# Kernel optimization log

Measured on AMD Instinct MI355X. Metric: run time of the kernel, lower is better.

The kernel has to match this reference:

```python
import jax, jax.numpy as jnp
import numpy as np

HIDDEN_DIM = 2048
NUM_HEADS = 16
HEAD_DIM = HIDDEN_DIM // NUM_HEADS
BATCH = 2
SEQ = 2048


def setup_inputs() -> dict:
    key = jax.random.key(0)
    ks = jax.random.split(key, 5)
    scale = 1.0 / np.sqrt(HIDDEN_DIM)
    x = jax.random.normal(ks[0], (BATCH, SEQ, HIDDEN_DIM), dtype=jnp.float32)
    w_q = jax.random.normal(ks[1], (HIDDEN_DIM, HIDDEN_DIM), dtype=jnp.float32) * scale
    w_k = jax.random.normal(ks[2], (HIDDEN_DIM, HIDDEN_DIM), dtype=jnp.float32) * scale
    w_v = jax.random.normal(ks[3], (HIDDEN_DIM, HIDDEN_DIM), dtype=jnp.float32) * scale
    w_o = jax.random.normal(ks[4], (HIDDEN_DIM, HIDDEN_DIM), dtype=jnp.float32) * scale
    return {"x": x, "w_q": w_q, "w_k": w_k, "w_v": w_v, "w_o": w_o}


def reference(x, w_q, w_k, w_v, w_o):
    # Projections: x @ W.T  (weights stored as (out, in) like torch)
    q = jnp.einsum('bsd,ed->bse', x, w_q)
    k = jnp.einsum('bsd,ed->bse', x, w_k)
    v = jnp.einsum('bsd,ed->bse', x, w_v)
    b, s, _ = q.shape
    # split heads: (b, h, s, hd)
    q = q.reshape(b, s, NUM_HEADS, HEAD_DIM).transpose(0, 2, 1, 3)
    k = k.reshape(b, s, NUM_HEADS, HEAD_DIM).transpose(0, 2, 1, 3)
    v = v.reshape(b, s, NUM_HEADS, HEAD_DIM).transpose(0, 2, 1, 3)
    scale = 1.0 / np.sqrt(HEAD_DIM)
    # Online-softmax tiling in the source (causal=False default) is
    # mathematically identical to standard softmax attention.
    scores = jnp.einsum('bhqd,bhkd->bhqk', q, k) * scale
    p = jax.nn.softmax(scores, axis=-1)
    o = jnp.einsum('bhqk,bhkd->bhqd', p, v)
    o = o.transpose(0, 2, 1, 3).reshape(b, s, HIDDEN_DIM)
    return jnp.einsum('bsd,ed->bse', o, w_o)
```

## Files before the change

### kernel.cpp

```cpp
#include <hip/hip_runtime.h>


typedef _Float16 half8 __attribute__((ext_vector_type(8)));
typedef float floatx4 __attribute__((ext_vector_type(4)));

__device__ __forceinline__ void async16(const void* g, void* l) {
  __builtin_amdgcn_global_load_lds((__attribute__((address_space(1))) void*)(g),
                                   (__attribute__((address_space(3))) void*)(l),
                                   16, 0, 0);
}

__global__ void cvt_f32_f16(const float* __restrict__ src, _Float16* __restrict__ dst,
                            int n4) {
  int i = blockIdx.x * blockDim.x + threadIdx.x;
  if (i >= n4) return;
  float4 v = reinterpret_cast<const float4*>(src)[i];
  union { _Float16 h[4]; short4 s; } u;
  u.h[0] = (_Float16)v.x; u.h[1] = (_Float16)v.y;
  u.h[2] = (_Float16)v.z; u.h[3] = (_Float16)v.w;
  reinterpret_cast<short4*>(dst)[i] = u.s;
}

__global__ void cvt_w4(const float* __restrict__ w0, const float* __restrict__ w1,
                       const float* __restrict__ w2, const float* __restrict__ w3,
                       _Float16* __restrict__ dst, float scale0) {
  int i = blockIdx.x * blockDim.x + threadIdx.x;
  int m = i >> 20, j = i & ((1 << 20) - 1);
  const float* src = (m == 0) ? w0 : (m == 1) ? w1 : (m == 2) ? w2 : w3;
  float sc = (m == 0) ? scale0 : 1.0f;
  float4 v = reinterpret_cast<const float4*>(src)[j];
  union { _Float16 h[4]; short4 s; } u;
  u.h[0] = (_Float16)(v.x * sc); u.h[1] = (_Float16)(v.y * sc);
  u.h[2] = (_Float16)(v.z * sc); u.h[3] = (_Float16)(v.w * sc);
  reinterpret_cast<short4*>(dst)[i] = u.s;
}

template <int OUT_MODE>
__global__ __launch_bounds__(256)
void gemm_nt(const _Float16* __restrict__ A, const _Float16* __restrict__ Bw,
             void* __restrict__ Cv, void* __restrict__ Cv2, int K) {
  __shared__ _Float16 As[128 * 64];
  __shared__ _Float16 Bs[128 * 64];
  const int tid = threadIdx.x;
  const int wave = tid >> 6, lane = tid & 63;
  const int wm = wave >> 1, wn = wave & 1;
  const int l15 = lane & 15, l4 = lane >> 4;
  const int bm = blockIdx.y, bn = blockIdx.x;

  floatx4 acc[4][4] = {};

  for (int k0 = 0; k0 < K; k0 += 64) {
    __syncthreads();
#pragma unroll
    for (int i = 0; i < 4; ++i) {
      int c = i * 256 + tid;
      int row = c >> 3, cc = c & 7;
      int g = cc ^ (row & 7);
      async16(A + (size_t)(bm * 128 + row) * K + k0 + g * 8, &As[c * 8]);
      async16(Bw + (size_t)(bn * 128 + row) * K + k0 + g * 8, &Bs[c * 8]);
    }
    __syncthreads();
#pragma unroll
    for (int ks = 0; ks < 2; ++ks) {
      half8 af[4], bf[4];
#pragma unroll
      for (int t = 0; t < 4; ++t) {
        int ra = wm * 64 + t * 16 + l15;
        int rb = wn * 64 + t * 16 + l15;
        int ch = (ks * 4 + l4) ^ (l15 & 7);
        af[t] = *reinterpret_cast<const half8*>(&As[ra * 64 + ch * 8]);
        bf[t] = *reinterpret_cast<const half8*>(&Bs[rb * 64 + ch * 8]);
      }
#pragma unroll
      for (int mt = 0; mt < 4; ++mt)
#pragma unroll
        for (int nt = 0; nt < 4; ++nt)
          acc[mt][nt] = __builtin_amdgcn_mfma_f32_16x16x32_f16(af[mt], bf[nt], acc[mt][nt], 0, 0, 0);
    }
  }

  const int rbase = bm * 128 + wm * 64;
  const int cbase = bn * 128 + wn * 64;
  if constexpr (OUT_MODE == 0) {
    if (cbase < 4096) {
      _Float16* C = (_Float16*)Cv + (size_t)(cbase >> 11) * (4096ull * 2048);
#pragma unroll
      for (int mt = 0; mt < 4; ++mt)
#pragma unroll
        for (int nt = 0; nt < 4; ++nt) {
          int r0 = rbase + mt * 16 + l4 * 4;
          int cg = (cbase + nt * 16 + l15) & 2047;
#pragma unroll
          for (int r = 0; r < 4; ++r)
            C[(size_t)(r0 + r) * 2048 + cg] = (_Float16)acc[mt][nt][r];
        }
    } else {
      _Float16* C = (_Float16*)Cv2;
#pragma unroll
      for (int mt = 0; mt < 4; ++mt)
#pragma unroll
        for (int nt = 0; nt < 4; ++nt) {
          int m0 = rbase + mt * 16 + l4 * 4;
          int d = cbase + nt * 16 + l15 - 4096;
          size_t base = (size_t)(m0 >> 11) * (2048ull * 2048) + (size_t)d * 2048 + (m0 & 2047);
          union { _Float16 h[4]; short4 s; } u;
#pragma unroll
          for (int r = 0; r < 4; ++r) u.h[r] = (_Float16)acc[mt][nt][r];
          *reinterpret_cast<short4*>(C + base) = u.s;
        }
    }
  } else {
    float* C = (float*)Cv;
#pragma unroll
    for (int mt = 0; mt < 4; ++mt)
#pragma unroll
      for (int nt = 0; nt < 4; ++nt) {
        int r0 = rbase + mt * 16 + l4 * 4;
        int cg = cbase + nt * 16 + l15;
#pragma unroll
        for (int r = 0; r < 4; ++r)
          C[(size_t)(r0 + r) * 2048 + cg] = acc[mt][nt][r];
      }
  }
}

__global__ __launch_bounds__(256, 4)
void flash_attn(const _Float16* __restrict__ Q, const _Float16* __restrict__ Kg,
                const _Float16* __restrict__ Vt, _Float16* __restrict__ O) {
  __shared__ _Float16 Ks[64 * 128];
  __shared__ _Float16 Vs[128 * 64];
  __shared__ _Float16 Ps[64 * 64];
  const int tid = threadIdx.x, wave = tid >> 6, lane = tid & 63;
  const int l15 = lane & 15, l4 = lane >> 4;
  const int bh = blockIdx.y, b = bh >> 4, h = bh & 15;
  const int q0 = blockIdx.x * 64;

  const _Float16* Qp = Q + ((size_t)(b * 2048 + q0 + wave * 16)) * 2048 + h * 128;
  const _Float16* Kp = Kg + (size_t)b * 2048 * 2048 + h * 128;
  const _Float16* Vp = Vt + (size_t)b * 2048 * 2048 + (size_t)(h * 128) * 2048;

  half8 qf[4];
#pragma unroll
  for (int ks = 0; ks < 4; ++ks)
    qf[ks] = *reinterpret_cast<const half8*>(Qp + (size_t)l15 * 2048 + ks * 32 + l4 * 8);

  floatx4 oacc[8] = {};
  float lsum[4] = {0.f, 0.f, 0.f, 0.f};

  for (int k0 = 0; k0 < 2048; k0 += 64) {
    __syncthreads();
#pragma unroll
    for (int i = 0; i < 4; ++i) {
      int c = i * 256 + tid;
      int row = c >> 4, cc = c & 15;
      int g = cc ^ (row & 15);
      async16(Kp + (size_t)(k0 + row) * 2048 + g * 8, &Ks[c * 8]);
    }
#pragma unroll
    for (int i = 0; i < 4; ++i) {
      int c = i * 256 + tid;
      int row = c >> 3, cc = c & 7;
      int g = cc ^ (row & 7);
      async16(Vp + (size_t)row * 2048 + k0 + g * 8, &Vs[c * 8]);
    }
    __syncthreads();

    floatx4 sacc[4] = {};
#pragma unroll
    for (int ks = 0; ks < 4; ++ks) {
      half8 bf[4];
#pragma unroll
      for (int nt = 0; nt < 4; ++nt) {
        int row = nt * 16 + l15;
        int ch = (ks * 4 + l4) ^ l15;
        bf[nt] = *reinterpret_cast<const half8*>(&Ks[row * 128 + ch * 8]);
      }
#pragma unroll
      for (int nt = 0; nt < 4; ++nt)
        sacc[nt] = __builtin_amdgcn_mfma_f32_16x16x32_f16(qf[ks], bf[nt], sacc[nt], 0, 0, 0);
    }

#pragma unroll
    for (int nt = 0; nt < 4; ++nt)
#pragma unroll
      for (int r = 0; r < 4; ++r) {
        float p = exp2f(sacc[nt][r]);
        lsum[r] += p;
        int rl = l4 * 4 + r;
        int ch = (nt * 2 + (l15 >> 3)) ^ (rl & 7);
        Ps[(wave * 16 + rl) * 64 + ch * 8 + (l15 & 7)] = (_Float16)p;
      }

    __builtin_amdgcn_s_waitcnt(0xC07F);

#pragma unroll
    for (int ks2 = 0; ks2 < 2; ++ks2) {
      half8 pf = *reinterpret_cast<const half8*>(
          &Ps[(wave * 16 + l15) * 64 + (((ks2 * 4 + l4) ^ (l15 & 7)) * 8)]);
#pragma unroll
      for (int nt2 = 0; nt2 < 8; ++nt2) {
        int row = nt2 * 16 + l15;
        int ch = (ks2 * 4 + l4) ^ (row & 7);
        half8 vf = *reinterpret_cast<const half8*>(&Vs[row * 64 + ch * 8]);
        oacc[nt2] = __builtin_amdgcn_mfma_f32_16x16x32_f16(pf, vf, oacc[nt2], 0, 0, 0);
      }
    }
  }

#pragma unroll
  for (int r = 0; r < 4; ++r) {
#pragma unroll
    for (int off = 1; off < 16; off <<= 1) lsum[r] += __shfl_xor(lsum[r], off);
  }

  _Float16* Op = O + ((size_t)(b * 2048 + q0 + wave * 16)) * 2048 + h * 128;
#pragma unroll
  for (int r = 0; r < 4; ++r) {
    float inv = 1.0f / lsum[r];
#pragma unroll
    for (int nt2 = 0; nt2 < 8; ++nt2) {
      int row = l4 * 4 + r;
      int col = nt2 * 16 + l15;
      Op[(size_t)row * 2048 + col] = (_Float16)(oacc[nt2][r] * inv);
    }
  }
}

extern "C" void kernel_launch(void* const* d_in, const int* in_sizes, int n_in,
                              void* d_out, int out_size, void* d_ws, size_t ws_size,
                              hipStream_t stream) {
  const float* x = (const float*)d_in[0];
  const float* wq = (const float*)d_in[1];
  const float* wk = (const float*)d_in[2];
  const float* wv = (const float*)d_in[3];
  const float* wo = (const float*)d_in[4];
  float* out = (float*)d_out;

  const size_t XN = (size_t)4096 * 2048;
  const size_t WN = (size_t)2048 * 2048;
  _Float16* xh = (_Float16*)d_ws;
  _Float16* qh = xh + XN;
  _Float16* vth = xh + 3 * XN;
  _Float16* oh = xh + 4 * XN;
  _Float16* wqh = xh + 5 * XN;

  const float SM_SCALE = 0.08838834764831845f * 1.4426950408889634f;

  cvt_f32_f16<<<dim3((int)(XN / 4 / 256)), 256, 0, stream>>>(x, xh, (int)(XN / 4));
  cvt_w4<<<dim3((int)(4 * WN / 4 / 256)), 256, 0, stream>>>(wq, wk, wv, wo, wqh, SM_SCALE);

  gemm_nt<0><<<dim3(48, 32), 256, 0, stream>>>(xh, wqh, qh, vth, 2048);
  flash_attn<<<dim3(32, 32), 256, 0, stream>>>(qh, qh + XN, vth, oh);
  gemm_nt<2><<<dim3(16, 32), 256, 0, stream>>>(oh, wqh + 3 * WN, out, nullptr, 2048);
}
```

Baseline: 422.7 us.

## Double query rows per attention wave and shrink output GEMM tile

Each flash-attention wave now processes 32 query rows instead of 16. Every K and V tile loaded into LDS therefore feeds twice as many MFMAs, and the grid halves to 512 blocks. The output projection GEMM is templated to a 128x64 tile with 4-wave occupancy, doubling its grid to 1024 blocks so the 256 CUs stay better filled. The cost is higher register pressure in attention (occupancy hint lowered to 2), which may reduce latency hiding.

Result: faster. 406.2 us (-3.9%).

```diff
diff --git a/kernel.cpp b/kernel.cpp
--- a/kernel.cpp
+++ b/kernel.cpp
@@ -35,59 +35,66 @@
   reinterpret_cast<short4*>(dst)[i] = u.s;
 }
 
-template <int OUT_MODE>
-__global__ __launch_bounds__(256)
+template <int OUT_MODE, int BM, int BN, int MINW>
+__global__ __launch_bounds__(256, MINW)
 void gemm_nt(const _Float16* __restrict__ A, const _Float16* __restrict__ Bw,
              void* __restrict__ Cv, void* __restrict__ Cv2, int K) {
-  __shared__ _Float16 As[128 * 64];
-  __shared__ _Float16 Bs[128 * 64];
+  constexpr int MT = BM / 32;
+  constexpr int NT = BN / 32;
+  __shared__ _Float16 As[BM * 64];
+  __shared__ _Float16 Bs[BN * 64];
   const int tid = threadIdx.x;
   const int wave = tid >> 6, lane = tid & 63;
   const int wm = wave >> 1, wn = wave & 1;
   const int l15 = lane & 15, l4 = lane >> 4;
   const int bm = blockIdx.y, bn = blockIdx.x;
 
-  floatx4 acc[4][4] = {};
+  floatx4 acc[MT][NT] = {};
 
   for (int k0 = 0; k0 < K; k0 += 64) {
     __syncthreads();
 #pragma unroll
-    for (int i = 0; i < 4; ++i) {
+    for (int i = 0; i < BM * 8 / 256; ++i) {
       int c = i * 256 + tid;
       int row = c >> 3, cc = c & 7;
       int g = cc ^ (row & 7);
-      async16(A + (size_t)(bm * 128 + row) * K + k0 + g * 8, &As[c * 8]);
-      async16(Bw + (size_t)(bn * 128 + row) * K + k0 + g * 8, &Bs[c * 8]);
+      async16(A + (size_t)(bm * BM + row) * K + k0 + g * 8, &As[c * 8]);
+    }
+#pragma unroll
+    for (int i = 0; i < BN * 8 / 256; ++i) {
+      int c = i * 256 + tid;
+      int row = c >> 3, cc = c & 7;
+      int g = cc ^ (row & 7);
+      async16(Bw + (size_t)(bn * BN + row) * K + k0 + g * 8, &Bs[c * 8]);
     }
     __syncthreads();
 #pragma unroll
     for (int ks = 0; ks < 2; ++ks) {
-      half8 af[4], bf[4];
-#pragma unroll
-      for (int t = 0; t < 4; ++t) {
-        int ra = wm * 64 + t * 16 + l15;
-        int rb = wn * 64 + t * 16 + l15;
-        int ch = (ks * 4 + l4) ^ (l15 & 7);
-        af[t] = *reinterpret_cast<const half8*>(&As[ra * 64 + ch * 8]);
-        bf[t] = *reinterpret_cast<const half8*>(&Bs[rb * 64 + ch * 8]);
-      }
-#pragma unroll
-      for (int mt = 0; mt < 4; ++mt)
-#pragma unroll
-        for (int nt = 0; nt < 4; ++nt)
+      half8 af[MT], bf[NT];
+      int ch = (ks * 4 + l4) ^ (l15 & 7);
+#pragma unroll
+      for (int t = 0; t < MT; ++t)
+        af[t] = *reinterpret_cast<const half8*>(&As[(wm * (BM / 2) + t * 16 + l15) * 64 + ch * 8]);
+#pragma unroll
+      for (int t = 0; t < NT; ++t)
+        bf[t] = *reinterpret_cast<const half8*>(&Bs[(wn * (BN / 2) + t * 16 + l15) * 64 + ch * 8]);
+#pragma unroll
+      for (int mt = 0; mt < MT; ++mt)
+#pragma unroll
+        for (int nt = 0; nt < NT; ++nt)
           acc[mt][nt] = __builtin_amdgcn_mfma_f32_16x16x32_f16(af[mt], bf[nt], acc[mt][nt], 0, 0, 0);
     }
   }
 
-  const int rbase = bm * 128 + wm * 64;
-  const int cbase = bn * 128 + wn * 64;
+  const int rbase = bm * BM + wm * (BM / 2);
+  const int cbase = bn * BN + wn * (BN / 2);
   if constexpr (OUT_MODE == 0) {
     if (cbase < 4096) {
       _Float16* C = (_Float16*)Cv + (size_t)(cbase >> 11) * (4096ull * 2048);
 #pragma unroll
-      for (int mt = 0; mt < 4; ++mt)
-#pragma unroll
-        for (int nt = 0; nt < 4; ++nt) {
+      for (int mt = 0; mt < MT; ++mt)
+#pragma unroll
+        for (int nt = 0; nt < NT; ++nt) {
           int r0 = rbase + mt * 16 + l4 * 4;
           int cg = (cbase + nt * 16 + l15) & 2047;
 #pragma unroll
@@ -97,9 +104,9 @@
     } else {
       _Float16* C = (_Float16*)Cv2;
 #pragma unroll
-      for (int mt = 0; mt < 4; ++mt)
-#pragma unroll
-        for (int nt = 0; nt < 4; ++nt) {
+      for (int mt = 0; mt < MT; ++mt)
+#pragma unroll
+        for (int nt = 0; nt < NT; ++nt) {
           int m0 = rbase + mt * 16 + l4 * 4;
           int d = cbase + nt * 16 + l15 - 4096;
           size_t base = (size_t)(m0 >> 11) * (2048ull * 2048) + (size_t)d * 2048 + (m0 & 2047);
@@ -112,9 +119,9 @@
   } else {
     float* C = (float*)Cv;
 #pragma unroll
-    for (int mt = 0; mt < 4; ++mt)
-#pragma unroll
-      for (int nt = 0; nt < 4; ++nt) {
+    for (int mt = 0; mt < MT; ++mt)
+#pragma unroll
+      for (int nt = 0; nt < NT; ++nt) {
         int r0 = rbase + mt * 16 + l4 * 4;
         int cg = cbase + nt * 16 + l15;
 #pragma unroll
@@ -124,28 +131,31 @@
   }
 }
 
-__global__ __launch_bounds__(256, 4)
+__global__ __launch_bounds__(256, 2)
 void flash_attn(const _Float16* __restrict__ Q, const _Float16* __restrict__ Kg,
                 const _Float16* __restrict__ Vt, _Float16* __restrict__ O) {
   __shared__ _Float16 Ks[64 * 128];
   __shared__ _Float16 Vs[128 * 64];
-  __shared__ _Float16 Ps[64 * 64];
+  __shared__ _Float16 Ps[128 * 64];
   const int tid = threadIdx.x, wave = tid >> 6, lane = tid & 63;
   const int l15 = lane & 15, l4 = lane >> 4;
   const int bh = blockIdx.y, b = bh >> 4, h = bh & 15;
-  const int q0 = blockIdx.x * 64;
-
-  const _Float16* Qp = Q + ((size_t)(b * 2048 + q0 + wave * 16)) * 2048 + h * 128;
+  const int q0 = blockIdx.x * 128;
+
+  const _Float16* Qp = Q + ((size_t)(b * 2048 + q0 + wave * 32)) * 2048 + h * 128;
   const _Float16* Kp = Kg + (size_t)b * 2048 * 2048 + h * 128;
   const _Float16* Vp = Vt + (size_t)b * 2048 * 2048 + (size_t)(h * 128) * 2048;
 
-  half8 qf[4];
-#pragma unroll
-  for (int ks = 0; ks < 4; ++ks)
-    qf[ks] = *reinterpret_cast<const half8*>(Qp + (size_t)l15 * 2048 + ks * 32 + l4 * 8);
-
-  floatx4 oacc[8] = {};
-  float lsum[4] = {0.f, 0.f, 0.f, 0.f};
+  half8 qf[2][4];
+#pragma unroll
+  for (int mt = 0; mt < 2; ++mt)
+#pragma unroll
+    for (int ks = 0; ks < 4; ++ks)
+      qf[mt][ks] = *reinterpret_cast<const half8*>(
+          Qp + (size_t)(mt * 16 + l15) * 2048 + ks * 32 + l4 * 8);
+
+  floatx4 oacc[2][8] = {};
+  float lsum[2][4] = {};
 
   for (int k0 = 0; k0 < 2048; k0 += 64) {
     __syncthreads();
@@ -165,7 +175,7 @@
     }
     __syncthreads();
 
-    floatx4 sacc[4] = {};
+    floatx4 sacc[2][4] = {};
 #pragma unroll
     for (int ks = 0; ks < 4; ++ks) {
       half8 bf[4];
@@ -176,54 +186,67 @@
         bf[nt] = *reinterpret_cast<const half8*>(&Ks[row * 128 + ch * 8]);
       }
 #pragma unroll
+      for (int mt = 0; mt < 2; ++mt)
+#pragma unroll
+        for (int nt = 0; nt < 4; ++nt)
+          sacc[mt][nt] = __builtin_amdgcn_mfma_f32_16x16x32_f16(qf[mt][ks], bf[nt], sacc[mt][nt], 0, 0, 0);
+    }
+
+#pragma unroll
+    for (int mt = 0; mt < 2; ++mt)
+#pragma unroll
       for (int nt = 0; nt < 4; ++nt)
-        sacc[nt] = __builtin_amdgcn_mfma_f32_16x16x32_f16(qf[ks], bf[nt], sacc[nt], 0, 0, 0);
-    }
-
-#pragma unroll
-    for (int nt = 0; nt < 4; ++nt)
-#pragma unroll
-      for (int r = 0; r < 4; ++r) {
-        float p = exp2f(sacc[nt][r]);
-        lsum[r] += p;
-        int rl = l4 * 4 + r;
-        int ch = (nt * 2 + (l15 >> 3)) ^ (rl & 7);
-        Ps[(wave * 16 + rl) * 64 + ch * 8 + (l15 & 7)] = (_Float16)p;
-      }
+#pragma unroll
+        for (int r = 0; r < 4; ++r) {
+          float p = exp2f(sacc[mt][nt][r]);
+          lsum[mt][r] += p;
+          int rl = l4 * 4 + r;
+          int ch = (nt * 2 + (l15 >> 3)) ^ (rl & 7);
+          Ps[(wave * 32 + mt * 16 + rl) * 64 + ch * 8 + (l15 & 7)] = (_Float16)p;
+        }
 
     __builtin_amdgcn_s_waitcnt(0xC07F);
 
 #pragma unroll
     for (int ks2 = 0; ks2 < 2; ++ks2) {
-      half8 pf = *reinterpret_cast<const half8*>(
-          &Ps[(wave * 16 + l15) * 64 + (((ks2 * 4 + l4) ^ (l15 & 7)) * 8)]);
+      half8 pf[2];
+#pragma unroll
+      for (int mt = 0; mt < 2; ++mt)
+        pf[mt] = *reinterpret_cast<const half8*>(
+            &Ps[(wave * 32 + mt * 16 + l15) * 64 + (((ks2 * 4 + l4) ^ (l15 & 7)) * 8)]);
 #pragma unroll
       for (int nt2 = 0; nt2 < 8; ++nt2) {
         int row = nt2 * 16 + l15;
         int ch = (ks2 * 4 + l4) ^ (row & 7);
         half8 vf = *reinterpret_cast<const half8*>(&Vs[row * 64 + ch * 8]);
-        oacc[nt2] = __builtin_amdgcn_mfma_f32_16x16x32_f16(pf, vf, oacc[nt2], 0, 0, 0);
+#pragma unroll
+        for (int mt = 0; mt < 2; ++mt)
+          oacc[mt][nt2] = __builtin_amdgcn_mfma_f32_16x16x32_f16(pf[mt], vf, oacc[mt][nt2], 0, 0, 0);
       }
     }
   }
 
 #pragma unroll
-  for (int r = 0; r < 4; ++r) {
-#pragma unroll
-    for (int off = 1; off < 16; off <<= 1) lsum[r] += __shfl_xor(lsum[r], off);
-  }
-
-  _Float16* Op = O + ((size_t)(b * 2048 + q0 + wave * 16)) * 2048 + h * 128;
-#pragma unroll
-  for (int r = 0; r < 4; ++r) {
-    float inv = 1.0f / lsum[r];
-#pragma unroll
-    for (int nt2 = 0; nt2 < 8; ++nt2) {
-      int row = l4 * 4 + r;
-      int col = nt2 * 16 + l15;
-      Op[(size_t)row * 2048 + col] = (_Float16)(oacc[nt2][r] * inv);
-    }
-  }
+  for (int mt = 0; mt < 2; ++mt)
+#pragma unroll
+    for (int r = 0; r < 4; ++r) {
+#pragma unroll
+      for (int off = 1; off < 16; off <<= 1) lsum[mt][r] += __shfl_xor(lsum[mt][r], off);
+    }
+
+  _Float16* Op = O + ((size_t)(b * 2048 + q0 + wave * 32)) * 2048 + h * 128;
+#pragma unroll
+  for (int mt = 0; mt < 2; ++mt)
+#pragma unroll
+    for (int r = 0; r < 4; ++r) {
+      float inv = 1.0f / lsum[mt][r];
+#pragma unroll
+      for (int nt2 = 0; nt2 < 8; ++nt2) {
+        int row = mt * 16 + l4 * 4 + r;
+        int col = nt2 * 16 + l15;
+        Op[(size_t)row * 2048 + col] = (_Float16)(oacc[mt][nt2][r] * inv);
+      }
+    }
 }
 
 extern "C" void kernel_launch(void* const* d_in, const int* in_sizes, int n_in,
@@ -249,7 +272,7 @@
   cvt_f32_f16<<<dim3((int)(XN / 4 / 256)), 256, 0, stream>>>(x, xh, (int)(XN / 4));
   cvt_w4<<<dim3((int)(4 * WN / 4 / 256)), 256, 0, stream>>>(wq, wk, wv, wo, wqh, SM_SCALE);
 
-  gemm_nt<0><<<dim3(48, 32), 256, 0, stream>>>(xh, wqh, qh, vth, 2048);
-  flash_attn<<<dim3(32, 32), 256, 0, stream>>>(qh, qh + XN, vth, oh);
-  gemm_nt<2><<<dim3(16, 32), 256, 0, stream>>>(oh, wqh + 3 * WN, out, nullptr, 2048);
-}
+  gemm_nt<0, 128, 128, 1><<<dim3(48, 32), 256, 0, stream>>>(xh, wqh, qh, vth, 2048);
+  flash_attn<<<dim3(16, 32), 256, 0, stream>>>(qh, qh + XN, vth, oh);
+  gemm_nt<2, 128, 64, 4><<<dim3(32, 32), 256, 0, stream>>>(oh, wqh + 3 * WN, out, nullptr, 2048);
+}
```
